# Kernel tuning notes

Measured on AMD Instinct MI355X. Metric: run time of the kernel, lower is better.

The kernel has to match this reference:

```python
import jax, jax.numpy as jnp
import numpy as np

NUM_EXPERTS = 8
TOP_K = 2

def setup_inputs() -> dict:
    key = jax.random.key(0)
    k1, k2, k3, k4 = jax.random.split(key, 4)
    B, L, D, F, E = 2, 2048, 1024, 2048, NUM_EXPERTS
    layer_input = jax.random.normal(k1, (B, L, D), dtype=jnp.float32)
    router_w = jax.random.normal(k2, (E, D), dtype=jnp.float32) * 0.02
    # input_linear.weight.transpose(2,1) in torch -> [E, D, 2F] layout here
    w1 = jax.random.normal(k3, (E, D, 2 * F), dtype=jnp.float32) * 0.02
    # output_linear.weight.transpose(2,1) -> [E, F, D]
    w2 = jax.random.normal(k4, (E, F, D), dtype=jnp.float32) * 0.02
    return {"layer_input": layer_input, "router_w": router_w, "w1": w1, "w2": w2}


def reference(layer_input, router_w, w1, w2):
    B, L, D = layer_input.shape
    E = router_w.shape[0]
    x = layer_input.reshape(-1, D)                              # [N, D]
    router_logits = x @ router_w.T                              # [N, E]
    probs = jax.nn.softmax(router_logits.astype(jnp.float32), axis=-1)
    routing_weights, selected = jax.lax.top_k(probs, TOP_K)     # [N, K]
    routing_weights = routing_weights / routing_weights.sum(-1, keepdims=True)
    routing_weights = routing_weights.astype(x.dtype)

    out = jnp.zeros_like(x)
    # Fixed small loop over experts; same math as sorted grouped-GEMM + scatter-combine.
    for e in range(E):
        gate_e = jnp.sum(jnp.where(selected == e, routing_weights, 0.0), axis=-1)  # [N]
        gh = x @ w1[e]                                          # [N, 2F]
        g, h = jnp.split(gh, 2, axis=-1)
        y = (jax.nn.silu(g) * h) @ w2[e]                        # [N, D]
        out = out + gate_e[:, None] * y
    return out.reshape(B, L, D)
```

## Files before the change

kernel.cpp:

```cpp
#include <hip/hip_runtime.h>
#include <stdint.h>

typedef unsigned short u16;
typedef __attribute__((ext_vector_type(8))) short short8;
typedef __attribute__((ext_vector_type(4))) float floatx4;

#define NTOK 4096
#define DDIM 1024
#define FDIM 2048
#define NEXP 8

__device__ __forceinline__ u16 f2bf(float f) {
    union { float f; uint32_t u; } v; v.f = f;
    uint32_t r = v.u + 0x7fff + ((v.u >> 16) & 1);
    return (u16)(r >> 16);
}
__device__ __forceinline__ uint32_t pk2(float a, float b) {
    return (uint32_t)f2bf(a) | ((uint32_t)f2bf(b) << 16);
}
__device__ __forceinline__ void gl_lds16(const u16* g, u16* l) {
    __builtin_amdgcn_global_load_lds(
        (const __attribute__((address_space(1))) uint32_t*)g,
        (__attribute__((address_space(3))) uint32_t*)l, 16, 0, 0);
}

__global__ __launch_bounds__(256)
void router_kernel(const float* __restrict__ x, const float* __restrict__ rw,
                   int* __restrict__ topk_e, float* __restrict__ topk_w,
                   u16* __restrict__ xb) {
    const int lane = threadIdx.x & 63;
    const int wv = threadIdx.x >> 6;
    const int tok = blockIdx.x * 4 + wv;
    const float* xr = x + (size_t)tok * DDIM;
    u16* xo = xb + (size_t)tok * DDIM;
    float acc[8];
#pragma unroll
    for (int e = 0; e < 8; ++e) acc[e] = 0.f;
#pragma unroll
    for (int it = 0; it < 4; ++it) {
        int d0 = (it * 64 + lane) * 4;
        float4 xv = *(const float4*)(xr + d0);
        uint2 o = { pk2(xv.x, xv.y), pk2(xv.z, xv.w) };
        *(uint2*)(xo + d0) = o;
#pragma unroll
        for (int e = 0; e < 8; ++e) {
            float4 wv4 = *(const float4*)(rw + (size_t)e * DDIM + d0);
            acc[e] += xv.x * wv4.x + xv.y * wv4.y + xv.z * wv4.z + xv.w * wv4.w;
        }
    }
#pragma unroll
    for (int s = 32; s > 0; s >>= 1)
#pragma unroll
        for (int e = 0; e < 8; ++e) acc[e] += __shfl_down(acc[e], s);
    if (lane == 0) {
        int e0 = 0;
#pragma unroll
        for (int e = 1; e < 8; ++e) if (acc[e] > acc[e0]) e0 = e;
        int e1 = (e0 == 0) ? 1 : 0;
#pragma unroll
        for (int e = 0; e < 8; ++e) if (e != e0 && acc[e] > acc[e1]) e1 = e;
        float w0 = 1.f / (1.f + __expf(acc[e1] - acc[e0]));
        topk_e[tok * 2 + 0] = e0;
        topk_e[tok * 2 + 1] = e1;
        topk_w[tok * 2 + 0] = w0;
        topk_w[tok * 2 + 1] = 1.f - w0;
    }
}

__global__ __launch_bounds__(256)
void prefix_kernel(const int* __restrict__ topk_e, int* __restrict__ counts,
                   int* __restrict__ offs, int* __restrict__ cursors) {
    __shared__ int h[NEXP];
    const int t = threadIdx.x;
    if (t < NEXP) h[t] = 0;
    __syncthreads();
    int c[NEXP];
#pragma unroll
    for (int j = 0; j < NEXP; ++j) c[j] = 0;
    const int4* te4 = (const int4*)topk_e;
#pragma unroll
    for (int it = 0; it < 8; ++it) {
        int4 v = te4[it * 256 + t];
#pragma unroll
        for (int j = 0; j < NEXP; ++j)
            c[j] += (v.x == j) + (v.y == j) + (v.z == j) + (v.w == j);
    }
#pragma unroll
    for (int j = 0; j < NEXP; ++j)
        if (c[j]) atomicAdd(&h[j], c[j]);
    __syncthreads();
    if (t == 0) {
        int s = 0;
        for (int e = 0; e < NEXP; ++e) {
            counts[e] = h[e];
            offs[e] = s;
            s += h[e];
        }
        offs[NEXP] = s;
    }
    if (t < NEXP) cursors[t] = 0;
}

__global__ __launch_bounds__(256)
void build_rows(const int* __restrict__ topk_e, const int* __restrict__ offs,
                int* __restrict__ cursors, int* __restrict__ row_tok,
                int* __restrict__ tok_row) {
    __shared__ int lcnt[NEXP];
    __shared__ int lbase[NEXP];
    const int t = threadIdx.x;
    if (t < NEXP) lcnt[t] = 0;
    __syncthreads();
    const int tok = blockIdx.x * 256 + t;
    const int e0 = topk_e[tok * 2 + 0];
    const int e1 = topk_e[tok * 2 + 1];
    const int s0 = atomicAdd(&lcnt[e0], 1);
    const int s1 = atomicAdd(&lcnt[e1], 1);
    __syncthreads();
    if (t < NEXP) lbase[t] = lcnt[t] ? atomicAdd(&cursors[t], lcnt[t]) : 0;
    __syncthreads();
    int r0 = offs[e0] + lbase[e0] + s0;
    row_tok[r0] = tok;
    tok_row[tok * 2 + 0] = r0;
    int r1 = offs[e1] + lbase[e1] + s1;
    row_tok[r1] = tok;
    tok_row[tok * 2 + 1] = r1;
}

__global__ __launch_bounds__(256)
void transpose_f32_bf16(const float* __restrict__ src, u16* __restrict__ dst,
                        int R, int C) {
    __shared__ float tile[64][65];
    size_t eo = (size_t)blockIdx.z * R * C;
    const float* S = src + eo;
    u16* D = dst + eo;
    int r0 = blockIdx.y * 64, c0 = blockIdx.x * 64;
    int t = threadIdx.x;
    int rr = t >> 4;
    int cc = (t & 15) * 4;
#pragma unroll
    for (int it = 0; it < 4; ++it) {
        int r = rr + it * 16;
        float4 v = *(const float4*)(S + (size_t)(r0 + r) * C + (c0 + cc));
        tile[cc + 0][r] = v.x; tile[cc + 1][r] = v.y;
        tile[cc + 2][r] = v.z; tile[cc + 3][r] = v.w;
    }
    __syncthreads();
#pragma unroll
    for (int it = 0; it < 2; ++it) {
        int u = it * 256 + t;
        int c = u >> 3;
        int rv = (u & 7) * 8;
        uint4 o;
        o.x = pk2(tile[c][rv + 0], tile[c][rv + 1]);
        o.y = pk2(tile[c][rv + 2], tile[c][rv + 3]);
        o.z = pk2(tile[c][rv + 4], tile[c][rv + 5]);
        o.w = pk2(tile[c][rv + 6], tile[c][rv + 7]);
        *(uint4*)(D + (size_t)(c0 + c) * R + (r0 + rv)) = o;
    }
}

__global__ __launch_bounds__(256, 2)
void gemm1_fast(const u16* __restrict__ xb, const u16* __restrict__ w1b,
                u16* __restrict__ act, const int* __restrict__ row_tok,
                const int* __restrict__ counts, const int* __restrict__ offs) {
    const int bid = blockIdx.x;
    const int e = bid & 7;
    const int cnt = counts[e];
    const int nmb = (cnt + 127) >> 7;
    const int j = bid >> 3;
    if (j >= nmb * 32) return;
    const int m0 = (j % nmb) * 128;
    const int n0 = (j / nmb) * 64;
    const int off = offs[e];

    __shared__ __align__(16) u16 As[2 * 128 * 32];
    __shared__ __align__(16) u16 Bs[2 * 128 * 32];

    const int t = threadIdx.x;
    const int lane = t & 63;
    const int wv = t >> 6;
    const int quad = lane >> 4;
    const int rr = lane & 15;
    const int wm = (wv & 1) * 64;
    const int wn = (wv >> 1) * 32;

    const int scol = (((lane & 3) ^ ((lane >> 3) & 3)) * 8);
    const int xq = (quad ^ ((rr >> 1) & 3)) * 8;
    const u16* arA[2];
    const u16* arB[2];
#pragma unroll
    for (int i = 0; i < 2; ++i) {
        int m = wv * 32 + i * 16 + ((lane >> 2) & 15);
        int r = m0 + m; if (r >= cnt) r = cnt - 1;
        arA[i] = xb + (size_t)row_tok[off + r] * DDIM + scol;
        size_t brow = (m < 64) ? ((size_t)e * 4096 + n0 + m)
                               : ((size_t)e * 4096 + 2048 + n0 + (m - 64));
        arB[i] = w1b + brow * DDIM + scol;
    }
    u16* dstA[2][2];
    u16* dstB[2][2];
#pragma unroll
    for (int s = 0; s < 2; ++s)
#pragma unroll
        for (int i = 0; i < 2; ++i) {
            dstA[s][i] = &As[(s * 128 + wv * 32 + i * 16) * 32];
            dstB[s][i] = &Bs[(s * 128 + wv * 32 + i * 16) * 32];
        }

    floatx4 accg[4][2] = {};
    floatx4 acch[4][2] = {};

    for (int k0 = 0; k0 < DDIM; k0 += 64) {
        __syncthreads();
#pragma unroll
        for (int s = 0; s < 2; ++s)
#pragma unroll
            for (int i = 0; i < 2; ++i) {
                gl_lds16(arA[i] + k0 + s * 32, dstA[s][i]);
                gl_lds16(arB[i] + k0 + s * 32, dstB[s][i]);
            }
        __syncthreads();

#pragma unroll
        for (int s = 0; s < 2; ++s) {
            short8 af[4], bg[2], bh[2];
#pragma unroll
            for (int mt = 0; mt < 4; ++mt)
                af[mt] = *(const short8*)&As[(s * 128 + wm + mt * 16 + rr) * 32 + xq];
#pragma unroll
            for (int nt = 0; nt < 2; ++nt) {
                bg[nt] = *(const short8*)&Bs[(s * 128 + wn + nt * 16 + rr) * 32 + xq];
                bh[nt] = *(const short8*)&Bs[(s * 128 + 64 + wn + nt * 16 + rr) * 32 + xq];
            }
#pragma unroll
            for (int mt = 0; mt < 4; ++mt)
#pragma unroll
                for (int nt = 0; nt < 2; ++nt) {
                    accg[mt][nt] = __builtin_amdgcn_mfma_f32_16x16x32_bf16(af[mt], bg[nt], accg[mt][nt], 0, 0, 0);
                    acch[mt][nt] = __builtin_amdgcn_mfma_f32_16x16x32_bf16(af[mt], bh[nt], acch[mt][nt], 0, 0, 0);
                }
        }
    }
#pragma unroll
    for (int mt = 0; mt < 4; ++mt)
#pragma unroll
        for (int nt = 0; nt < 2; ++nt)
#pragma unroll
            for (int rg = 0; rg < 4; ++rg) {
                int gm = m0 + wm + mt * 16 + quad * 4 + rg;
                if (gm < cnt) {
                    float g = accg[mt][nt][rg];
                    float h = acch[mt][nt][rg];
                    float s = g / (1.f + __expf(-g));
                    act[(size_t)(off + gm) * FDIM + (n0 + wn + nt * 16 + rr)] = f2bf(s * h);
                }
            }
}

__global__ __launch_bounds__(256, 2)
void gemm2_fast(const u16* __restrict__ act, const u16* __restrict__ w2b,
                float* __restrict__ y, const int* __restrict__ counts,
                const int* __restrict__ offs) {
    const int bid = blockIdx.x;
    const int e = bid & 7;
    const int cnt = counts[e];
    const int nmb = (cnt + 127) >> 7;
    const int j = bid >> 3;
    if (j >= nmb * 8) return;
    const int m0 = (j % nmb) * 128;
    const int n0 = (j / nmb) * 128;
    const int off = offs[e];

    __shared__ __align__(16) u16 As[2 * 128 * 32];
    __shared__ __align__(16) u16 Bs[2 * 128 * 32];

    const int t = threadIdx.x;
    const int lane = t & 63;
    const int wv = t >> 6;
    const int quad = lane >> 4;
    const int rr = lane & 15;
    const int wm = (wv & 1) * 64;
    const int wn = (wv >> 1) * 64;

    const int scol = (((lane & 3) ^ ((lane >> 3) & 3)) * 8);
    const int xq = (quad ^ ((rr >> 1) & 3)) * 8;
    const u16* arA[2];
    const u16* arB[2];
#pragma unroll
    for (int i = 0; i < 2; ++i) {
        int m = wv * 32 + i * 16 + ((lane >> 2) & 15);
        int r = m0 + m; if (r >= cnt) r = cnt - 1;
        arA[i] = act + (size_t)(off + r) * FDIM + scol;
        arB[i] = w2b + ((size_t)e * 1024 + n0 + m) * FDIM + scol;
    }
    u16* dstA[2][2];
    u16* dstB[2][2];
#pragma unroll
    for (int s = 0; s < 2; ++s)
#pragma unroll
        for (int i = 0; i < 2; ++i) {
            dstA[s][i] = &As[(s * 128 + wv * 32 + i * 16) * 32];
            dstB[s][i] = &Bs[(s * 128 + wv * 32 + i * 16) * 32];
        }

    floatx4 acc[4][4] = {};

    for (int k0 = 0; k0 < FDIM; k0 += 64) {
        __syncthreads();
#pragma unroll
        for (int s = 0; s < 2; ++s)
#pragma unroll
            for (int i = 0; i < 2; ++i) {
                gl_lds16(arA[i] + k0 + s * 32, dstA[s][i]);
                gl_lds16(arB[i] + k0 + s * 32, dstB[s][i]);
            }
        __syncthreads();

#pragma unroll
        for (int s = 0; s < 2; ++s) {
            short8 af[4], bf[4];
#pragma unroll
            for (int mt = 0; mt < 4; ++mt)
                af[mt] = *(const short8*)&As[(s * 128 + wm + mt * 16 + rr) * 32 + xq];
#pragma unroll
            for (int nt = 0; nt < 4; ++nt)
                bf[nt] = *(const short8*)&Bs[(s * 128 + wn + nt * 16 + rr) * 32 + xq];
#pragma unroll
            for (int mt = 0; mt < 4; ++mt)
#pragma unroll
                for (int nt = 0; nt < 4; ++nt)
                    acc[mt][nt] = __builtin_amdgcn_mfma_f32_16x16x32_bf16(af[mt], bf[nt], acc[mt][nt], 0, 0, 0);
        }
    }
#pragma unroll
    for (int mt = 0; mt < 4; ++mt)
#pragma unroll
        for (int rg = 0; rg < 4; ++rg) {
            int gm = m0 + wm + mt * 16 + quad * 4 + rg;
            if (gm < cnt) {
                float* yrow = y + (size_t)(off + gm) * DDIM + n0 + wn;
#pragma unroll
                for (int nt = 0; nt < 4; ++nt)
                    yrow[nt * 16 + rr] = acc[mt][nt][rg];
            }
        }
}

__global__ __launch_bounds__(256)
void combine_kernel(const float* __restrict__ y, const int* __restrict__ tok_row,
                    const float* __restrict__ topk_w, float* __restrict__ out) {
    const int tok = blockIdx.x;
    const int t = threadIdx.x;
    const int r0 = tok_row[tok * 2 + 0];
    const int r1 = tok_row[tok * 2 + 1];
    const float w0 = topk_w[tok * 2 + 0];
    const float w1 = topk_w[tok * 2 + 1];
    float4 a = *(const float4*)(y + (size_t)r0 * DDIM + t * 4);
    float4 b = *(const float4*)(y + (size_t)r1 * DDIM + t * 4);
    float4 o = { w0 * a.x + w1 * b.x, w0 * a.y + w1 * b.y,
                 w0 * a.z + w1 * b.z, w0 * a.w + w1 * b.w };
    *(float4*)(out + (size_t)tok * DDIM + t * 4) = o;
}

extern "C" void kernel_launch(void* const* d_in, const int* in_sizes, int n_in,
                              void* d_out, int out_size, void* d_ws, size_t ws_size,
                              hipStream_t stream) {
    const float* x  = (const float*)d_in[0];
    const float* rw = (const float*)d_in[1];
    const float* w1 = (const float*)d_in[2];
    const float* w2 = (const float*)d_in[3];
    float* out = (float*)d_out;

    char* ws = (char*)d_ws;
    const size_t MB = 1ull << 20;
    int*   counts   = (int*)(ws);
    int*   cursors  = (int*)(ws + 64);
    int*   offs     = (int*)(ws + 128);
    int*   topk_e   = (int*)(ws + 2048);
    float* topk_w   = (float*)(ws + 2048 + 32768);
    int*   row_tok  = (int*)(ws + 2048 + 65536);
    int*   tok_row  = (int*)(ws + 2048 + 98304);
    u16*   act      = (u16*)(ws + 1 * MB);
    u16*   xb       = (u16*)(ws + 33 * MB);
    u16*   w1b      = (u16*)(ws + 41 * MB);
    u16*   w2b      = (u16*)(ws + 41 * MB);
    float* yb       = (float*)(ws + 73 * MB);

    router_kernel<<<dim3(NTOK / 4), 256, 0, stream>>>(x, rw, topk_e, topk_w, xb);
    prefix_kernel<<<1, 256, 0, stream>>>(topk_e, counts, offs, cursors);
    build_rows<<<dim3(NTOK / 256), 256, 0, stream>>>(topk_e, offs, cursors, row_tok, tok_row);
    transpose_f32_bf16<<<dim3(4096 / 64, 1024 / 64, NEXP), 256, 0, stream>>>(w1, w1b, 1024, 4096);
    gemm1_fast<<<dim3(8192), 256, 0, stream>>>(xb, w1b, act, row_tok, counts, offs);
    transpose_f32_bf16<<<dim3(1024 / 64, 2048 / 64, NEXP), 256, 0, stream>>>(w2, w2b, 2048, 1024);
    gemm2_fast<<<dim3(2048), 256, 0, stream>>>(act, w2b, yb, counts, offs);
    combine_kernel<<<dim3(NTOK), 256, 0, stream>>>(yb, tok_row, topk_w, out);
    (void)in_sizes; (void)n_in; (void)ws_size;
}
```

Before: 431.4 us.

## Merge routing prefix and row build into one kernel; split gemm1 into two launches

```diff
diff --git a/kernel.cpp b/kernel.cpp
--- a/kernel.cpp
+++ b/kernel.cpp
@@ -68,62 +68,58 @@
 }
 
 __global__ __launch_bounds__(256)
-void prefix_kernel(const int* __restrict__ topk_e, int* __restrict__ counts,
-                   int* __restrict__ offs, int* __restrict__ cursors) {
-    __shared__ int h[NEXP];
+void build_rows_all(const int* __restrict__ topk_e, int* __restrict__ counts,
+                    int* __restrict__ offs, int* __restrict__ row_tok,
+                    int* __restrict__ tok_row) {
+    __shared__ int h[NEXP], hb[NEXP], lcnt[NEXP], loffs[NEXP];
     const int t = threadIdx.x;
-    if (t < NEXP) h[t] = 0;
+    const int B = blockIdx.x;
+    if (t < NEXP) { h[t] = 0; hb[t] = 0; lcnt[t] = 0; }
     __syncthreads();
-    int c[NEXP];
-#pragma unroll
-    for (int j = 0; j < NEXP; ++j) c[j] = 0;
+    int cf[NEXP], cb[NEXP];
+#pragma unroll
+    for (int j = 0; j < NEXP; ++j) { cf[j] = 0; cb[j] = 0; }
     const int4* te4 = (const int4*)topk_e;
+    const int gb = B * 128;
 #pragma unroll
     for (int it = 0; it < 8; ++it) {
-        int4 v = te4[it * 256 + t];
-#pragma unroll
-        for (int j = 0; j < NEXP; ++j)
-            c[j] += (v.x == j) + (v.y == j) + (v.z == j) + (v.w == j);
-    }
-#pragma unroll
-    for (int j = 0; j < NEXP; ++j)
-        if (c[j]) atomicAdd(&h[j], c[j]);
+        int g = it * 256 + t;
+        int4 v = te4[g];
+        int before = (g < gb);
+#pragma unroll
+        for (int j = 0; j < NEXP; ++j) {
+            int m = (v.x == j) + (v.y == j) + (v.z == j) + (v.w == j);
+            cf[j] += m;
+            cb[j] += before ? m : 0;
+        }
+    }
+#pragma unroll
+    for (int j = 0; j < NEXP; ++j) {
+        if (cf[j]) atomicAdd(&h[j], cf[j]);
+        if (cb[j]) atomicAdd(&hb[j], cb[j]);
+    }
     __syncthreads();
     if (t == 0) {
         int s = 0;
-        for (int e = 0; e < NEXP; ++e) {
-            counts[e] = h[e];
-            offs[e] = s;
-            s += h[e];
-        }
-        offs[NEXP] = s;
-    }
-    if (t < NEXP) cursors[t] = 0;
-}
-
-__global__ __launch_bounds__(256)
-void build_rows(const int* __restrict__ topk_e, const int* __restrict__ offs,
-                int* __restrict__ cursors, int* __restrict__ row_tok,
-                int* __restrict__ tok_row) {
-    __shared__ int lcnt[NEXP];
-    __shared__ int lbase[NEXP];
-    const int t = threadIdx.x;
-    if (t < NEXP) lcnt[t] = 0;
+        for (int e = 0; e < NEXP; ++e) { loffs[e] = s; s += h[e]; }
+    }
     __syncthreads();
-    const int tok = blockIdx.x * 256 + t;
+    const int tok = B * 256 + t;
     const int e0 = topk_e[tok * 2 + 0];
     const int e1 = topk_e[tok * 2 + 1];
     const int s0 = atomicAdd(&lcnt[e0], 1);
     const int s1 = atomicAdd(&lcnt[e1], 1);
-    __syncthreads();
-    if (t < NEXP) lbase[t] = lcnt[t] ? atomicAdd(&cursors[t], lcnt[t]) : 0;
-    __syncthreads();
-    int r0 = offs[e0] + lbase[e0] + s0;
+    int r0 = loffs[e0] + hb[e0] + s0;
     row_tok[r0] = tok;
     tok_row[tok * 2 + 0] = r0;
-    int r1 = offs[e1] + lbase[e1] + s1;
+    int r1 = loffs[e1] + hb[e1] + s1;
     row_tok[r1] = tok;
     tok_row[tok * 2 + 1] = r1;
+    if (B == 0 && t < NEXP) {
+        counts[t] = h[t];
+        offs[t] = loffs[t];
+        if (t == 0) offs[NEXP] = loffs[NEXP - 1] + h[NEXP - 1];
+    }
 }
 
 __global__ __launch_bounds__(256)
@@ -162,15 +158,16 @@
 __global__ __launch_bounds__(256, 2)
 void gemm1_fast(const u16* __restrict__ xb, const u16* __restrict__ w1b,
                 u16* __restrict__ act, const int* __restrict__ row_tok,
-                const int* __restrict__ counts, const int* __restrict__ offs) {
+                const int* __restrict__ counts, const int* __restrict__ offs,
+                int nhalf) {
     const int bid = blockIdx.x;
     const int e = bid & 7;
     const int cnt = counts[e];
     const int nmb = (cnt + 127) >> 7;
     const int j = bid >> 3;
-    if (j >= nmb * 32) return;
+    if (j >= nmb * 16) return;
     const int m0 = (j % nmb) * 128;
-    const int n0 = (j / nmb) * 64;
+    const int n0 = (j / nmb + nhalf * 16) * 64;
     const int off = offs[e];
 
     __shared__ __align__(16) u16 As[2 * 128 * 32];
@@ -374,7 +371,6 @@
     char* ws = (char*)d_ws;
     const size_t MB = 1ull << 20;
     int*   counts   = (int*)(ws);
-    int*   cursors  = (int*)(ws + 64);
     int*   offs     = (int*)(ws + 128);
     int*   topk_e   = (int*)(ws + 2048);
     float* topk_w   = (float*)(ws + 2048 + 32768);
@@ -387,10 +383,10 @@
     float* yb       = (float*)(ws + 73 * MB);
 
     router_kernel<<<dim3(NTOK / 4), 256, 0, stream>>>(x, rw, topk_e, topk_w, xb);
-    prefix_kernel<<<1, 256, 0, stream>>>(topk_e, counts, offs, cursors);
-    build_rows<<<dim3(NTOK / 256), 256, 0, stream>>>(topk_e, offs, cursors, row_tok, tok_row);
+    build_rows_all<<<dim3(NTOK / 256), 256, 0, stream>>>(topk_e, counts, offs, row_tok, tok_row);
     transpose_f32_bf16<<<dim3(4096 / 64, 1024 / 64, NEXP), 256, 0, stream>>>(w1, w1b, 1024, 4096);
-    gemm1_fast<<<dim3(8192), 256, 0, stream>>>(xb, w1b, act, row_tok, counts, offs);
+    gemm1_fast<<<dim3(4096), 256, 0, stream>>>(xb, w1b, act, row_tok, counts, offs, 0);
+    gemm1_fast<<<dim3(4096), 256, 0, stream>>>(xb, w1b, act, row_tok, counts, offs, 1);
     transpose_f32_bf16<<<dim3(1024 / 64, 2048 / 64, NEXP), 256, 0, stream>>>(w2, w2b, 2048, 1024);
     gemm2_fast<<<dim3(2048), 256, 0, stream>>>(act, w2b, yb, counts, offs);
     combine_kernel<<<dim3(NTOK), 256, 0, stream>>>(yb, tok_row, topk_w, out);
```

New measurement: 452.2 us. 4.8% more time.

## Enlarge gemm1 tiles and add a three-stage async LDS pipeline

Applied to the files above, without the earlier changes.

```diff
diff --git a/kernel.cpp b/kernel.cpp
--- a/kernel.cpp
+++ b/kernel.cpp
@@ -23,6 +23,13 @@
         (const __attribute__((address_space(1))) uint32_t*)g,
         (__attribute__((address_space(3))) uint32_t*)l, 16, 0, 0);
 }
+
+#define WAITV8 asm volatile("s_waitcnt vmcnt(8)" ::: "memory")
+#define WAITV4 asm volatile("s_waitcnt vmcnt(4)" ::: "memory")
+#define WAITV0 asm volatile("s_waitcnt vmcnt(0)" ::: "memory")
+#define LGKM0  asm volatile("s_waitcnt lgkmcnt(0)" ::: "memory")
+#define BAR    __builtin_amdgcn_s_barrier()
+#define CFENCE asm volatile("" ::: "memory")
 
 __global__ __launch_bounds__(256)
 void router_kernel(const float* __restrict__ x, const float* __restrict__ rw,
@@ -159,100 +166,106 @@
     }
 }
 
-__global__ __launch_bounds__(256, 2)
+__global__ __launch_bounds__(512, 2)
 void gemm1_fast(const u16* __restrict__ xb, const u16* __restrict__ w1b,
                 u16* __restrict__ act, const int* __restrict__ row_tok,
                 const int* __restrict__ counts, const int* __restrict__ offs) {
     const int bid = blockIdx.x;
     const int e = bid & 7;
     const int cnt = counts[e];
-    const int nmb = (cnt + 127) >> 7;
+    const int nmb = (cnt + 255) >> 8;
     const int j = bid >> 3;
-    if (j >= nmb * 32) return;
-    const int m0 = (j % nmb) * 128;
-    const int n0 = (j / nmb) * 64;
+    if (j >= nmb * 16) return;
+    const int m0 = (j % nmb) * 256;
+    const int n0 = (j / nmb) * 128;
     const int off = offs[e];
 
-    __shared__ __align__(16) u16 As[2 * 128 * 32];
-    __shared__ __align__(16) u16 Bs[2 * 128 * 32];
+    __shared__ __align__(16) u16 As[3 * 256 * 32];
+    __shared__ __align__(16) u16 Bs[3 * 256 * 32];
 
     const int t = threadIdx.x;
     const int lane = t & 63;
     const int wv = t >> 6;
     const int quad = lane >> 4;
     const int rr = lane & 15;
-    const int wm = (wv & 1) * 64;
-    const int wn = (wv >> 1) * 32;
+    const int wr = wv >> 2;
+    const int wc = wv & 3;
 
     const int scol = (((lane & 3) ^ ((lane >> 3) & 3)) * 8);
     const int xq = (quad ^ ((rr >> 1) & 3)) * 8;
+
     const u16* arA[2];
     const u16* arB[2];
 #pragma unroll
     for (int i = 0; i < 2; ++i) {
-        int m = wv * 32 + i * 16 + ((lane >> 2) & 15);
+        int m = wv * 32 + i * 16 + (lane >> 2);
         int r = m0 + m; if (r >= cnt) r = cnt - 1;
         arA[i] = xb + (size_t)row_tok[off + r] * DDIM + scol;
-        size_t brow = (m < 64) ? ((size_t)e * 4096 + n0 + m)
-                               : ((size_t)e * 4096 + 2048 + n0 + (m - 64));
+        int br = m;
+        int u = br & 63;
+        size_t brow = (size_t)e * 4096 + n0 + (br >> 6) * 32 + (u & 31)
+                      + ((u >= 32) ? 2048 : 0);
         arB[i] = w1b + brow * DDIM + scol;
     }
-    u16* dstA[2][2];
-    u16* dstB[2][2];
-#pragma unroll
-    for (int s = 0; s < 2; ++s)
-#pragma unroll
-        for (int i = 0; i < 2; ++i) {
-            dstA[s][i] = &As[(s * 128 + wv * 32 + i * 16) * 32];
-            dstB[s][i] = &Bs[(s * 128 + wv * 32 + i * 16) * 32];
-        }
-
-    floatx4 accg[4][2] = {};
-    floatx4 acch[4][2] = {};
-
-    for (int k0 = 0; k0 < DDIM; k0 += 64) {
-        __syncthreads();
-#pragma unroll
-        for (int s = 0; s < 2; ++s)
-#pragma unroll
-            for (int i = 0; i < 2; ++i) {
-                gl_lds16(arA[i] + k0 + s * 32, dstA[s][i]);
-                gl_lds16(arB[i] + k0 + s * 32, dstB[s][i]);
-            }
-        __syncthreads();
-
-#pragma unroll
-        for (int s = 0; s < 2; ++s) {
-            short8 af[4], bg[2], bh[2];
-#pragma unroll
-            for (int mt = 0; mt < 4; ++mt)
-                af[mt] = *(const short8*)&As[(s * 128 + wm + mt * 16 + rr) * 32 + xq];
-#pragma unroll
-            for (int nt = 0; nt < 2; ++nt) {
-                bg[nt] = *(const short8*)&Bs[(s * 128 + wn + nt * 16 + rr) * 32 + xq];
-                bh[nt] = *(const short8*)&Bs[(s * 128 + 64 + wn + nt * 16 + rr) * 32 + xq];
-            }
-#pragma unroll
-            for (int mt = 0; mt < 4; ++mt)
-#pragma unroll
-                for (int nt = 0; nt < 2; ++nt) {
-                    accg[mt][nt] = __builtin_amdgcn_mfma_f32_16x16x32_bf16(af[mt], bg[nt], accg[mt][nt], 0, 0, 0);
-                    acch[mt][nt] = __builtin_amdgcn_mfma_f32_16x16x32_bf16(af[mt], bh[nt], acch[mt][nt], 0, 0, 0);
-                }
-        }
-    }
-#pragma unroll
-    for (int mt = 0; mt < 4; ++mt)
+    u16* dA[2] = { &As[(wv * 32) * 32], &As[(wv * 32 + 16) * 32] };
+    u16* dB[2] = { &Bs[(wv * 32) * 32], &Bs[(wv * 32 + 16) * 32] };
+
+    floatx4 accg[8][2] = {};
+    floatx4 acch[8][2] = {};
+
+#define G1_STAGE(ss, tt)                                   \
+    { gl_lds16(arA[0] + (tt) * 32, dA[0] + (ss) * 8192);   \
+      gl_lds16(arA[1] + (tt) * 32, dA[1] + (ss) * 8192);   \
+      gl_lds16(arB[0] + (tt) * 32, dB[0] + (ss) * 8192);   \
+      gl_lds16(arB[1] + (tt) * 32, dB[1] + (ss) * 8192); }
+
+#define G1_COMPUTE(cs)                                                          \
+    { short8 af[8], bg[2], bh[2];                                               \
+      _Pragma("unroll") for (int mt = 0; mt < 8; ++mt)                          \
+          af[mt] = *(const short8*)&As[(cs) * 8192 + (wr * 128 + mt * 16 + rr) * 32 + xq]; \
+      _Pragma("unroll") for (int nt = 0; nt < 2; ++nt) {                        \
+          bg[nt] = *(const short8*)&Bs[(cs) * 8192 + (wc * 64 + nt * 16 + rr) * 32 + xq]; \
+          bh[nt] = *(const short8*)&Bs[(cs) * 8192 + (wc * 64 + 32 + nt * 16 + rr) * 32 + xq]; } \
+      _Pragma("unroll") for (int mt = 0; mt < 8; ++mt)                          \
+      _Pragma("unroll") for (int nt = 0; nt < 2; ++nt) {                        \
+          accg[mt][nt] = __builtin_amdgcn_mfma_f32_16x16x32_bf16(af[mt], bg[nt], accg[mt][nt], 0, 0, 0); \
+          acch[mt][nt] = __builtin_amdgcn_mfma_f32_16x16x32_bf16(af[mt], bh[nt], acch[mt][nt], 0, 0, 0); } }
+
+#define G1_BODY(tt, cs, ss)                                \
+    G1_STAGE(ss, (tt) + 2);                                \
+    WAITV8; BAR; CFENCE;                                   \
+    G1_COMPUTE(cs);                                        \
+    LGKM0; BAR; CFENCE;
+
+    G1_STAGE(0, 0);
+    G1_STAGE(1, 1);
+    CFENCE;
+    for (int tb = 0; tb < 30; tb += 3) {
+        G1_BODY(tb + 0, 0, 2);
+        G1_BODY(tb + 1, 1, 0);
+        G1_BODY(tb + 2, 2, 1);
+    }
+    WAITV4; BAR; CFENCE;
+    G1_COMPUTE(0);
+    LGKM0;
+    WAITV0; BAR; CFENCE;
+    G1_COMPUTE(1);
+#undef G1_STAGE
+#undef G1_COMPUTE
+#undef G1_BODY
+
+#pragma unroll
+    for (int mt = 0; mt < 8; ++mt)
 #pragma unroll
         for (int nt = 0; nt < 2; ++nt)
 #pragma unroll
             for (int rg = 0; rg < 4; ++rg) {
-                int gm = m0 + wm + mt * 16 + quad * 4 + rg;
+                int gm = m0 + wr * 128 + mt * 16 + quad * 4 + rg;
                 if (gm < cnt) {
                     float g = accg[mt][nt][rg];
                     float h = acch[mt][nt][rg];
                     float s = g / (1.f + __expf(-g));
-                    act[(size_t)(off + gm) * FDIM + (n0 + wn + nt * 16 + rr)] = f2bf(s * h);
+                    act[(size_t)(off + gm) * FDIM + (n0 + wc * 32 + nt * 16 + rr)] = f2bf(s * h);
                 }
             }
 }
@@ -390,7 +403,7 @@
     prefix_kernel<<<1, 256, 0, stream>>>(topk_e, counts, offs, cursors);
     build_rows<<<dim3(NTOK / 256), 256, 0, stream>>>(topk_e, offs, cursors, row_tok, tok_row);
     transpose_f32_bf16<<<dim3(4096 / 64, 1024 / 64, NEXP), 256, 0, stream>>>(w1, w1b, 1024, 4096);
-    gemm1_fast<<<dim3(8192), 256, 0, stream>>>(xb, w1b, act, row_tok, counts, offs);
+    gemm1_fast<<<dim3(2048), 512, 0, stream>>>(xb, w1b, act, row_tok, counts, offs);
     transpose_f32_bf16<<<dim3(1024 / 64, 2048 / 64, NEXP), 256, 0, stream>>>(w2, w2b, 2048, 1024);
     gemm2_fast<<<dim3(2048), 256, 0, stream>>>(act, w2b, yb, counts, offs);
     combine_kernel<<<dim3(NTOK), 256, 0, stream>>>(yb, tok_row, topk_w, out);
```

After: 451.3 us. 1.05x slower.
